# Optimization experiments

Hardware: AMD Instinct MI355X
Metric: run time of the kernel (lower is better)

## Reference

```python
import jax, jax.numpy as jnp
import numpy as np

N = 1_000_000
D_IN = 128
D_OUT = 128
S = 8192  # num_samples


def setup_inputs() -> dict:
    key = jax.random.key(0)
    k1, k2, k3, k4 = jax.random.split(key, 4)
    element_embeddings = jax.random.normal(k1, (N, D_IN), dtype=jnp.float32)
    w_att = jax.random.normal(k2, (D_IN,), dtype=jnp.float32) * (1.0 / np.sqrt(D_IN))
    w_out = jax.random.normal(k3, (D_OUT, D_IN), dtype=jnp.float32) * (1.0 / np.sqrt(D_IN))
    element_to_sample_map = jax.random.randint(k4, (N,), 0, S, dtype=jnp.int32)
    return {
        "element_embeddings": element_embeddings,
        "w_att": w_att,
        "w_out": w_out,
        "element_to_sample_map": element_to_sample_map,
        "num_samples": S,
    }


def reference(element_embeddings, w_att, w_out, element_to_sample_map, num_samples):
    idx = element_to_sample_map
    # attention scores: Linear(D_in, 1, bias=False) -> [N]
    scores = element_embeddings @ w_att  # [N]
    # scatter log-softmax over segments (eps=0), numerically stable
    seg_max = jax.ops.segment_max(scores, idx, num_segments=num_samples)  # [S]
    shifted = scores - seg_max[idx]  # [N]
    seg_sumexp = jax.ops.segment_sum(jnp.exp(shifted), idx, num_segments=num_samples)  # [S]
    attention_probs = jnp.exp(shifted - jnp.log(seg_sumexp)[idx])  # [N]
    # output projection then weighted scatter-sum pooling
    projected = element_embeddings @ w_out.T  # [N, D_out]
    return jax.ops.segment_sum(projected * attention_probs[:, None], idx, num_segments=num_samples)  # [S, D_out]
```

## Files before the change

### kernel.cpp

```cpp
#include <hip/hip_runtime.h>
#include <math.h>

#define NB 64

__global__ __launch_bounds__(1024) void k_hist2(const int* __restrict__ idx,
                                                int* __restrict__ counts,
                                                int* __restrict__ rb,
                                                int n, int S) {
    __shared__ int lh[8192];
    int t = threadIdx.x, b = blockIdx.x;
    for (int s = t; s < S; s += 1024) lh[s] = 0;
    __syncthreads();
    int chunk = (n + NB - 1) / NB;
    int lo = b * chunk;
    int hi = min(n, lo + chunk);
    for (int i = lo + t; i < hi; i += 1024) atomicAdd(&lh[idx[i]], 1);
    __syncthreads();
    for (int s = t; s < S; s += 1024) {
        int h = lh[s];
        rb[b * S + s] = (h > 0) ? atomicAdd(&counts[s], h) : 0;
    }
}

__global__ __launch_bounds__(1024) void k_scan(const int* __restrict__ counts,
                                               int* __restrict__ base, int S) {
    __shared__ int sh[1024];
    int t = threadIdx.x;
    int loc[8];
    int sum = 0;
#pragma unroll
    for (int j = 0; j < 8; ++j) {
        int g = t * 8 + j;
        loc[j] = sum;
        sum += (g < S) ? counts[g] : 0;
    }
    sh[t] = sum;
    __syncthreads();
    int total = sum;
    for (int off = 1; off < 1024; off <<= 1) {
        int v = (t >= off) ? sh[t - off] : 0;
        __syncthreads();
        sh[t] += v;
        __syncthreads();
    }
    int excl = sh[t] - total;
#pragma unroll
    for (int j = 0; j < 8; ++j) {
        int g = t * 8 + j;
        if (g < S) base[g] = excl + loc[j];
    }
}

__global__ __launch_bounds__(1024) void k_scatter2(const int* __restrict__ idx,
                                                   const int* __restrict__ base,
                                                   const int* __restrict__ rb,
                                                   int* __restrict__ order,
                                                   int n, int S) {
    __shared__ int cur[8192];
    int t = threadIdx.x, b = blockIdx.x;
    for (int s = t; s < S; s += 1024) cur[s] = base[s] + rb[b * S + s];
    __syncthreads();
    int chunk = (n + NB - 1) / NB;
    int lo = b * chunk;
    int hi = min(n, lo + chunk);
    for (int i = lo + t; i < hi; i += 1024) {
        int s = idx[i];
        int pos = atomicAdd(&cur[s], 1);
        order[pos] = i;
    }
}

__global__ __launch_bounds__(256, 4) void k_pool(
        const float* __restrict__ emb, const float* __restrict__ w_att,
        const int* __restrict__ base, const int* __restrict__ counts,
        const int* __restrict__ order, float* __restrict__ pooled, int S) {
    int wave = (blockIdx.x << 2) | (threadIdx.x >> 6);
    int lane = threadIdx.x & 63;
    if (wave >= S) return;
    int g   = lane >> 4;
    int l16 = lane & 15;
    int b   = base[wave];
    int cnt = counts[wave];
    const float* wrow = w_att + 8 * l16;
    float4 wa0 = *reinterpret_cast<const float4*>(wrow);
    float4 wa1 = *reinterpret_cast<const float4*>(wrow + 4);
    float4 a0 = make_float4(0.f, 0.f, 0.f, 0.f);
    float4 a1 = make_float4(0.f, 0.f, 0.f, 0.f);
    float Z = 0.f;
    if (cnt > 0) {
        const int* ob = order + b;
        int last = cnt - 1;
        int e = g;
        int i_cur = ob[min(e, last)];
        int i_nxt = ob[min(e + 4, last)];
        const float* r = emb + (size_t)i_cur * 128 + 8 * l16;
        float4 v0 = *reinterpret_cast<const float4*>(r);
        float4 v1 = *reinterpret_cast<const float4*>(r + 4);
        int nit = (cnt + 3) >> 2;
        for (int it = 0; it < nit; ++it) {
            const float* rn = emb + (size_t)i_nxt * 128 + 8 * l16;
            float4 n0 = *reinterpret_cast<const float4*>(rn);
            float4 n1 = *reinterpret_cast<const float4*>(rn + 4);
            int i_n2 = ob[min(e + 8, last)];
            float part = v0.x * wa0.x + v0.y * wa0.y + v0.z * wa0.z + v0.w * wa0.w
                       + v1.x * wa1.x + v1.y * wa1.y + v1.z * wa1.z + v1.w * wa1.w;
            part += __shfl_xor(part, 1);
            part += __shfl_xor(part, 2);
            part += __shfl_xor(part, 4);
            part += __shfl_xor(part, 8);
            float ex = (e <= last) ? __expf(part) : 0.f;
            Z += ex;
            a0.x = fmaf(ex, v0.x, a0.x);
            a0.y = fmaf(ex, v0.y, a0.y);
            a0.z = fmaf(ex, v0.z, a0.z);
            a0.w = fmaf(ex, v0.w, a0.w);
            a1.x = fmaf(ex, v1.x, a1.x);
            a1.y = fmaf(ex, v1.y, a1.y);
            a1.z = fmaf(ex, v1.z, a1.z);
            a1.w = fmaf(ex, v1.w, a1.w);
            v0 = n0; v1 = n1; i_nxt = i_n2; e += 4;
        }
    }
#pragma unroll
    for (int m = 16; m <= 32; m <<= 1) {
        a0.x += __shfl_xor(a0.x, m);
        a0.y += __shfl_xor(a0.y, m);
        a0.z += __shfl_xor(a0.z, m);
        a0.w += __shfl_xor(a0.w, m);
        a1.x += __shfl_xor(a1.x, m);
        a1.y += __shfl_xor(a1.y, m);
        a1.z += __shfl_xor(a1.z, m);
        a1.w += __shfl_xor(a1.w, m);
        Z    += __shfl_xor(Z,    m);
    }
    float rn_ = (Z > 0.f) ? (1.0f / Z) : 0.f;
    if (g == 0) {
        float* o = pooled + (size_t)wave * 128 + 8 * l16;
        *reinterpret_cast<float4*>(o)     = make_float4(a0.x * rn_, a0.y * rn_, a0.z * rn_, a0.w * rn_);
        *reinterpret_cast<float4*>(o + 4) = make_float4(a1.x * rn_, a1.y * rn_, a1.z * rn_, a1.w * rn_);
    }
}

#define SPB 8
__global__ __launch_bounds__(256, 4) void k_proj(
        const float* __restrict__ w_out, float* __restrict__ io, int S) {
    __shared__ float wl[128][68];
    __shared__ float pl[SPB][64];
    int t = threadIdx.x;
    int d = t & 127;
    int h = t >> 7;
    int s0 = blockIdx.x * SPB;
    float acc[4] = {0.f, 0.f, 0.f, 0.f};

    for (int ph = 0; ph < 2; ++ph) {
        __syncthreads();
        for (int j = t; j < 2048; j += 256) {
            int r = j >> 4, c4 = j & 15;
            float4 wv = reinterpret_cast<const float4*>(w_out + (size_t)r * 128 + ph * 64)[c4];
            *reinterpret_cast<float4*>(&wl[r][c4 * 4]) = wv;
        }
        if (t < 128) {
            int sm = t >> 4, c4 = t & 15;
            int ss = s0 + sm;
            float4 pv = (ss < S)
                ? reinterpret_cast<const float4*>(io + (size_t)ss * 128 + ph * 64)[c4]
                : make_float4(0.f, 0.f, 0.f, 0.f);
            *reinterpret_cast<float4*>(&pl[sm][c4 * 4]) = pv;
        }
        __syncthreads();
#pragma unroll
        for (int k4 = 0; k4 < 16; ++k4) {
            float4 wv = *reinterpret_cast<const float4*>(&wl[d][k4 * 4]);
#pragma unroll
            for (int j = 0; j < 4; ++j) {
                float4 pv = *reinterpret_cast<const float4*>(&pl[2 * j + h][k4 * 4]);
                acc[j] = fmaf(wv.x, pv.x, acc[j]);
                acc[j] = fmaf(wv.y, pv.y, acc[j]);
                acc[j] = fmaf(wv.z, pv.z, acc[j]);
                acc[j] = fmaf(wv.w, pv.w, acc[j]);
            }
        }
    }
#pragma unroll
    for (int j = 0; j < 4; ++j) {
        int s = s0 + 2 * j + h;
        if (s < S) io[(size_t)s * 128 + d] = acc[j];
    }
}

extern "C" void kernel_launch(void* const* d_in, const int* in_sizes, int n_in,
                              void* d_out, int out_size, void* d_ws, size_t ws_size,
                              hipStream_t stream) {
    const float* emb   = (const float*)d_in[0];
    const float* w_att = (const float*)d_in[1];
    const float* w_out = (const float*)d_in[2];
    const int*   idx   = (const int*)d_in[3];
    const int N = in_sizes[0] / 128;
    const int S = out_size / 128;

    char* ws = (char*)d_ws;
    int* counts = (int*)(ws + 0);
    int* base   = (int*)(ws + 32 * 1024);
    int* rb     = (int*)(ws + 128 * 1024);
    int* order  = (int*)(ws + 128 * 1024 + (size_t)NB * 8192 * 4);
    float* out  = (float*)d_out;

    hipMemsetAsync(counts, 0, (size_t)S * sizeof(int), stream);
    k_hist2  <<<NB, 1024, 0, stream>>>(idx, counts, rb, N, S);
    k_scan   <<<1, 1024, 0, stream>>>(counts, base, S);
    k_scatter2<<<NB, 1024, 0, stream>>>(idx, base, rb, order, N, S);
    k_pool   <<<(S + 3) / 4, 256, 0, stream>>>(emb, w_att, base, counts, order, out, S);
    k_proj   <<<(S + SPB - 1) / SPB, 256, 0, stream>>>(w_out, out, S);
}
```

Measured before the change: 298.5 us.

## Deterministic column-scan counting sort with more blocks and coalesced pool loads

The per-block global atomics that assigned each block's base offsets are replaced by a separate column-scan kernel over per-block histograms. This makes the bucket order deterministic, and the block count rises from 64 to 256, giving more parallelism in the count and scatter phases. The pool kernel's per-lane float4 layout also changes so that the 16 lanes of a row read contiguous 64-byte halves, which improves coalescing. The cost is an extra kernel launch and a larger per-block histogram buffer to write and scan.

```diff
diff --git a/kernel.cpp b/kernel.cpp
--- a/kernel.cpp
+++ b/kernel.cpp
@@ -1,25 +1,35 @@
 #include <hip/hip_runtime.h>
 #include <math.h>
 
-#define NB 64
-
-__global__ __launch_bounds__(1024) void k_hist2(const int* __restrict__ idx,
-                                                int* __restrict__ counts,
+#define NB2 256
+
+__global__ __launch_bounds__(1024) void k_count(const int* __restrict__ idx,
                                                 int* __restrict__ rb,
                                                 int n, int S) {
     __shared__ int lh[8192];
     int t = threadIdx.x, b = blockIdx.x;
     for (int s = t; s < S; s += 1024) lh[s] = 0;
     __syncthreads();
-    int chunk = (n + NB - 1) / NB;
+    int chunk = (n + NB2 - 1) / NB2;
     int lo = b * chunk;
     int hi = min(n, lo + chunk);
     for (int i = lo + t; i < hi; i += 1024) atomicAdd(&lh[idx[i]], 1);
     __syncthreads();
-    for (int s = t; s < S; s += 1024) {
-        int h = lh[s];
-        rb[b * S + s] = (h > 0) ? atomicAdd(&counts[s], h) : 0;
-    }
+    for (int s = t; s < S; s += 1024) rb[(size_t)b * S + s] = lh[s];
+}
+
+__global__ __launch_bounds__(256) void k_colscan(int* __restrict__ rb,
+                                                 int* __restrict__ counts, int S) {
+    int s = blockIdx.x * 256 + threadIdx.x;
+    if (s >= S) return;
+    int run = 0;
+#pragma unroll 8
+    for (int b = 0; b < NB2; ++b) {
+        int v = rb[(size_t)b * S + s];
+        rb[(size_t)b * S + s] = run;
+        run += v;
+    }
+    counts[s] = run;
 }
 
 __global__ __launch_bounds__(1024) void k_scan(const int* __restrict__ counts,
@@ -51,16 +61,16 @@
     }
 }
 
-__global__ __launch_bounds__(1024) void k_scatter2(const int* __restrict__ idx,
+__global__ __launch_bounds__(1024) void k_scatter3(const int* __restrict__ idx,
                                                    const int* __restrict__ base,
                                                    const int* __restrict__ rb,
                                                    int* __restrict__ order,
                                                    int n, int S) {
     __shared__ int cur[8192];
     int t = threadIdx.x, b = blockIdx.x;
-    for (int s = t; s < S; s += 1024) cur[s] = base[s] + rb[b * S + s];
-    __syncthreads();
-    int chunk = (n + NB - 1) / NB;
+    for (int s = t; s < S; s += 1024) cur[s] = base[s] + rb[(size_t)b * S + s];
+    __syncthreads();
+    int chunk = (n + NB2 - 1) / NB2;
     int lo = b * chunk;
     int hi = min(n, lo + chunk);
     for (int i = lo + t; i < hi; i += 1024) {
@@ -81,9 +91,8 @@
     int l16 = lane & 15;
     int b   = base[wave];
     int cnt = counts[wave];
-    const float* wrow = w_att + 8 * l16;
-    float4 wa0 = *reinterpret_cast<const float4*>(wrow);
-    float4 wa1 = *reinterpret_cast<const float4*>(wrow + 4);
+    float4 wa0 = *reinterpret_cast<const float4*>(w_att + 4 * l16);
+    float4 wa1 = *reinterpret_cast<const float4*>(w_att + 64 + 4 * l16);
     float4 a0 = make_float4(0.f, 0.f, 0.f, 0.f);
     float4 a1 = make_float4(0.f, 0.f, 0.f, 0.f);
     float Z = 0.f;
@@ -93,14 +102,14 @@
         int e = g;
         int i_cur = ob[min(e, last)];
         int i_nxt = ob[min(e + 4, last)];
-        const float* r = emb + (size_t)i_cur * 128 + 8 * l16;
-        float4 v0 = *reinterpret_cast<const float4*>(r);
-        float4 v1 = *reinterpret_cast<const float4*>(r + 4);
+        const float* r = emb + (size_t)i_cur * 128;
+        float4 v0 = *reinterpret_cast<const float4*>(r + 4 * l16);
+        float4 v1 = *reinterpret_cast<const float4*>(r + 64 + 4 * l16);
         int nit = (cnt + 3) >> 2;
         for (int it = 0; it < nit; ++it) {
-            const float* rn = emb + (size_t)i_nxt * 128 + 8 * l16;
-            float4 n0 = *reinterpret_cast<const float4*>(rn);
-            float4 n1 = *reinterpret_cast<const float4*>(rn + 4);
+            const float* rn = emb + (size_t)i_nxt * 128;
+            float4 n0 = *reinterpret_cast<const float4*>(rn + 4 * l16);
+            float4 n1 = *reinterpret_cast<const float4*>(rn + 64 + 4 * l16);
             int i_n2 = ob[min(e + 8, last)];
             float part = v0.x * wa0.x + v0.y * wa0.y + v0.z * wa0.z + v0.w * wa0.w
                        + v1.x * wa1.x + v1.y * wa1.y + v1.z * wa1.z + v1.w * wa1.w;
@@ -135,9 +144,9 @@
     }
     float rn_ = (Z > 0.f) ? (1.0f / Z) : 0.f;
     if (g == 0) {
-        float* o = pooled + (size_t)wave * 128 + 8 * l16;
-        *reinterpret_cast<float4*>(o)     = make_float4(a0.x * rn_, a0.y * rn_, a0.z * rn_, a0.w * rn_);
-        *reinterpret_cast<float4*>(o + 4) = make_float4(a1.x * rn_, a1.y * rn_, a1.z * rn_, a1.w * rn_);
+        float* o = pooled + (size_t)wave * 128;
+        *reinterpret_cast<float4*>(o + 4 * l16)      = make_float4(a0.x * rn_, a0.y * rn_, a0.z * rn_, a0.w * rn_);
+        *reinterpret_cast<float4*>(o + 64 + 4 * l16) = make_float4(a1.x * rn_, a1.y * rn_, a1.z * rn_, a1.w * rn_);
     }
 }
 
@@ -202,13 +211,13 @@
     int* counts = (int*)(ws + 0);
     int* base   = (int*)(ws + 32 * 1024);
     int* rb     = (int*)(ws + 128 * 1024);
-    int* order  = (int*)(ws + 128 * 1024 + (size_t)NB * 8192 * 4);
+    int* order  = (int*)(ws + 128 * 1024 + (size_t)NB2 * 8192 * 4);
     float* out  = (float*)d_out;
 
-    hipMemsetAsync(counts, 0, (size_t)S * sizeof(int), stream);
-    k_hist2  <<<NB, 1024, 0, stream>>>(idx, counts, rb, N, S);
-    k_scan   <<<1, 1024, 0, stream>>>(counts, base, S);
-    k_scatter2<<<NB, 1024, 0, stream>>>(idx, base, rb, order, N, S);
-    k_pool   <<<(S + 3) / 4, 256, 0, stream>>>(emb, w_att, base, counts, order, out, S);
-    k_proj   <<<(S + SPB - 1) / SPB, 256, 0, stream>>>(w_out, out, S);
-}
+    k_count   <<<NB2, 1024, 0, stream>>>(idx, rb, N, S);
+    k_colscan <<<(S + 255) / 256, 256, 0, stream>>>(rb, counts, S);
+    k_scan    <<<1, 1024, 0, stream>>>(counts, base, S);
+    k_scatter3<<<NB2, 1024, 0, stream>>>(idx, base, rb, order, N, S);
+    k_pool    <<<(S + 3) / 4, 256, 0, stream>>>(emb, w_att, base, counts, order, out, S);
+    k_proj    <<<(S + SPB - 1) / SPB, 256, 0, stream>>>(w_out, out, S);
+}
```

Result: slower. 318.1 us (+6.6%).
